# Kernel optimization log

Hardware: AMD Instinct MI355X
Metric: run time of the kernel (lower is better)

## Reference

```python
import jax, jax.numpy as jnp
import numpy as np

N = 100000
E = 300000
D = 128
EPS = 1e-5


def sage_conv(x, edge_index, Wl, bl, Wr):
    # PyG SAGEConv: out = lin_l(mean_{j in N(i)} x_j) + lin_r(x_i)
    src, dst = edge_index[0], edge_index[1]
    n = x.shape[0]
    agg = jax.ops.segment_sum(x[src], dst, num_segments=n)            # [N, d]
    cnt = jax.ops.segment_sum(jnp.ones((src.shape[0],), x.dtype), dst, num_segments=n)
    mean = agg / jnp.maximum(cnt, 1.0)[:, None]
    return mean @ Wl.T + bl + x @ Wr.T


def setup_inputs() -> dict:
    key = jax.random.key(0)
    ks = jax.random.split(key, 16)
    s = 0.05
    inp = {
        "feat": jax.random.normal(ks[0], (N, D), jnp.float32),
        "e0": jax.random.randint(ks[1], (2, E), 0, N, jnp.int32),
        "e1": jax.random.randint(ks[2], (2, E), 0, N, jnp.int32),
        "e2": jax.random.randint(ks[3], (2, E), 0, N, jnp.int32),
    }
    # per-etype SAGEConv params (in=hidden=128)
    for i, k in zip(range(3), (ks[4], ks[5], ks[6])):
        ka, kb = jax.random.split(k)
        inp[f"Wl{i}"] = jax.random.normal(ka, (D, D), jnp.float32) * s
        inp[f"bl{i}"] = jnp.zeros((D,), jnp.float32)
        inp[f"Wr{i}"] = jax.random.normal(kb, (D, D), jnp.float32) * s
    ka, kb = jax.random.split(ks[7])
    inp["Wla"] = jax.random.normal(ka, (D, D), jnp.float32) * s
    inp["bla"] = jnp.zeros((D,), jnp.float32)
    inp["Wra"] = jax.random.normal(kb, (D, D), jnp.float32) * s
    ka, kb = jax.random.split(ks[8])
    inp["Wf"] = jax.random.normal(ka, (D, D), jnp.float32) * s
    inp["bf"] = jnp.zeros((D,), jnp.float32)
    inp["Wrf"] = jax.random.normal(kb, (D, D), jnp.float32) * s
    inp["gamma"] = jnp.ones((D,), jnp.float32)
    inp["beta"] = jnp.zeros((D,), jnp.float32)
    inp["wt"] = jnp.ones((3,), jnp.float32)
    return inp


def reference(feat, Wl0, bl0, Wr0, Wl1, bl1, Wr1, Wl2, bl2, Wr2,
              Wla, bla, Wra, Wf, bf, Wrf, gamma, beta, wt, e0, e1, e2):
    out0 = sage_conv(feat, e0, Wl0, bl0, Wr0)
    out1 = sage_conv(feat, e1, Wl1, bl1, Wr1)
    out2 = sage_conv(feat, e2, Wl2, bl2, Wr2)
    all_e = jnp.concatenate([e0, e1, e2], axis=1)   # [2, 3E]
    all_out = sage_conv(feat, all_e, Wla, bla, Wra)
    comb = wt[0] * out0 + wt[1] * out1 + wt[2] * out2 + all_out
    comb = jax.nn.relu(comb)
    # BatchNorm1d (training mode: batch stats over node dim, biased var)
    mu = jnp.mean(comb, axis=0)
    var = jnp.mean((comb - mu) ** 2, axis=0)
    comb = (comb - mu) * jax.lax.rsqrt(var + EPS) * gamma + beta
    # dropout p=0.0 -> identity
    return sage_conv(comb, all_e, Wf, bf, Wrf)
```

## Files before the change

### kernel.cpp

```cpp
#include <hip/hip_runtime.h>

#define NN 100000
#define NE 300000
#define DD 128
#define NBLKG 782
#define NBLKSEG 49

typedef short bf16x8 __attribute__((ext_vector_type(8)));
typedef float f32x4 __attribute__((ext_vector_type(4)));
typedef unsigned u32x4 __attribute__((ext_vector_type(4)));

__device__ __forceinline__ unsigned short f2b(float f) {
    union { float f; unsigned u; } c; c.f = f;
    unsigned u = c.u;
    return (unsigned short)((u + 0x7fffu + ((u >> 16) & 1u)) >> 16);
}
__device__ __forceinline__ float b2lo(unsigned u) {
    union { float f; unsigned u; } c; c.u = u << 16; return c.f;
}
__device__ __forceinline__ float b2hi(unsigned u) {
    union { float f; unsigned u; } c; c.u = u & 0xffff0000u; return c.f;
}
__device__ __forceinline__ unsigned pack2(float lo, float hi) {
    return (unsigned)f2b(lo) | ((unsigned)f2b(hi) << 16);
}

__global__ __launch_bounds__(256) void feat_to_bf16(
    const float* __restrict__ feat, unsigned short* __restrict__ fb) {
    int gid = blockIdx.x * 256 + threadIdx.x;
    if (gid >= NN * 16) return;
    const f32x4* f4 = (const f32x4*)feat;
    f32x4 a = __builtin_nontemporal_load(&f4[gid * 2]);
    f32x4 b = __builtin_nontemporal_load(&f4[gid * 2 + 1]);
    uint4 o;
    o.x = pack2(a.x, a.y); o.y = pack2(a.z, a.w);
    o.z = pack2(b.x, b.y); o.w = pack2(b.z, b.w);
    ((uint4*)fb)[gid] = o;
}

__global__ __launch_bounds__(256) void prep_weights(
    const float* __restrict__ Wl0, const float* __restrict__ bl0, const float* __restrict__ Wr0,
    const float* __restrict__ Wl1, const float* __restrict__ bl1, const float* __restrict__ Wr1,
    const float* __restrict__ Wl2, const float* __restrict__ bl2, const float* __restrict__ Wr2,
    const float* __restrict__ Wla, const float* __restrict__ bla, const float* __restrict__ Wra,
    const float* __restrict__ Wf,  const float* __restrict__ bfv, const float* __restrict__ Wrf,
    const float* __restrict__ wt,
    unsigned short* __restrict__ WcatB, float* __restrict__ bias1,
    unsigned short* __restrict__ W2catB, float* __restrict__ bias2) {
    int idx = blockIdx.x * 256 + threadIdx.x;
    float w0 = wt[0], w1 = wt[1], w2 = wt[2];
    if (idx < 81920) {
        int f = idx / 640, k = idx % 640;
        float v;
        if (k < 128)      v = w0 * Wl0[f * 128 + k];
        else if (k < 256) v = w1 * Wl1[f * 128 + (k - 128)];
        else if (k < 384) v = w2 * Wl2[f * 128 + (k - 256)];
        else if (k < 512) v = Wla[f * 128 + (k - 384)];
        else {
            int kk = k - 512;
            v = w0 * Wr0[f * 128 + kk] + w1 * Wr1[f * 128 + kk] +
                w2 * Wr2[f * 128 + kk] + Wra[f * 128 + kk];
        }
        WcatB[idx] = f2b(v);
    } else if (idx < 81920 + 32768) {
        int j = idx - 81920;
        int f = j >> 8, k = j & 255;
        W2catB[j] = f2b((k < 128) ? Wf[f * 128 + k] : Wrf[f * 128 + (k - 128)]);
    } else if (idx < 81920 + 32768 + 128) {
        int f = idx - (81920 + 32768);
        bias1[f] = w0 * bl0[f] + w1 * bl1[f] + w2 * bl2[f] + bla[f];
        bias2[f] = bfv[f];
    }
}

__global__ __launch_bounds__(256) void count_deg(
    const int* __restrict__ e0, const int* __restrict__ e1, const int* __restrict__ e2,
    int* __restrict__ deg) {
    int gid = blockIdx.x * 256 + threadIdx.x;
    if (gid >= 3 * NE) return;
    int t = (gid < NE) ? 0 : ((gid < 2 * NE) ? 1 : 2);
    int i = gid - t * NE;
    const int* ep = (t == 0) ? e0 : ((t == 1) ? e1 : e2);
    atomicAdd(&deg[t * NN + ep[NE + i]], 1);
}

__global__ __launch_bounds__(256) void scan_local(
    const int* __restrict__ deg, int* __restrict__ rsloc, int* __restrict__ bsum) {
    __shared__ int sc[256];
    int b = blockIdx.x, tid = threadIdx.x;
    int seg = b / NBLKSEG, blk = b % NBLKSEG;
    int g0 = seg * NN;
    int base = blk * 2048 + tid * 8;
    int vals[8]; int tsum = 0;
#pragma unroll
    for (int j = 0; j < 8; ++j) {
        int l = base + j;
        int d = (l < NN) ? deg[g0 + l] : 0;
        vals[j] = tsum; tsum += d;
    }
    sc[tid] = tsum;
    __syncthreads();
    for (int off = 1; off < 256; off <<= 1) {
        int v = (tid >= off) ? sc[tid - off] : 0;
        __syncthreads();
        sc[tid] += v;
        __syncthreads();
    }
    int excl = sc[tid] - tsum;
#pragma unroll
    for (int j = 0; j < 8; ++j) {
        int l = base + j;
        if (l < NN) rsloc[g0 + l] = excl + vals[j];
    }
    if (tid == 255) bsum[b] = sc[255];
}

__global__ void scan_bsum(int* __restrict__ bsum) {
    int tid = threadIdx.x;
    if (tid < 3) {
        int run = 0;
        for (int b = 0; b < NBLKSEG; ++b) {
            int idx = tid * NBLKSEG + b;
            int t = bsum[idx]; bsum[idx] = run; run += t;
        }
    }
}

__global__ __launch_bounds__(256) void scan_fix(
    const int* __restrict__ deg, const int* __restrict__ rsloc, const int* __restrict__ bsum,
    int* __restrict__ fillpos, int* __restrict__ rowstartU, int* __restrict__ degall) {
    int blk = blockIdx.x, tid = threadIdx.x;
    int base = blk * 2048 + tid * 8;
    int o0 = bsum[blk], o1 = bsum[NBLKSEG + blk], o2 = bsum[2 * NBLKSEG + blk];
#pragma unroll
    for (int j = 0; j < 8; ++j) {
        int l = base + j;
        if (l < NN) {
            int d0 = deg[l], d1 = deg[NN + l], d2 = deg[2 * NN + l];
            int rU = (rsloc[l] + o0) + (rsloc[NN + l] + o1) + (rsloc[2 * NN + l] + o2);
            fillpos[l] = rU;
            fillpos[NN + l] = rU + d0;
            fillpos[2 * NN + l] = rU + d0 + d1;
            rowstartU[l] = rU;
            degall[l] = d0 + d1 + d2;
        }
    }
}

__global__ __launch_bounds__(256) void fill_csr(
    const int* __restrict__ e0, const int* __restrict__ e1, const int* __restrict__ e2,
    int* __restrict__ fillpos, int* __restrict__ csrU) {
    int gid = blockIdx.x * 256 + threadIdx.x;
    if (gid >= 3 * NE) return;
    int t = (gid < NE) ? 0 : ((gid < 2 * NE) ? 1 : 2);
    int i = gid - t * NE;
    const int* ep = (t == 0) ? e0 : ((t == 1) ? e1 : e2);
    int src = ep[i], dst = ep[NE + i];
    int p = atomicAdd(&fillpos[t * NN + dst], 1);
    csrU[p] = src;
}

__global__ __launch_bounds__(256) void gather1(
    const unsigned short* __restrict__ featB,
    const int* __restrict__ deg, const int* __restrict__ rowstartU,
    const int* __restrict__ degall, const int* __restrict__ csrU,
    unsigned short* __restrict__ meanB) {
    int n = __builtin_amdgcn_readfirstlane((int)((blockIdx.x * 256 + threadIdx.x) >> 6));
    if (n >= NN) return;
    int lane = threadIdx.x & 63;
    int d0 = deg[n], d1 = deg[NN + n];
    int dall = degall[n];
    int b1 = d0, b2 = d0 + d1;
    const int* cp = csrU + rowstartU[n];

    float p0 = 0.f, p1 = 0.f;
    float sA0 = 0.f, sA1 = 0.f;
    float sB0 = 0.f, sB1 = 0.f;

    unsigned f0 = 0, f1 = 0, f2 = 0, f3 = 0, f4 = 0;
    int i5 = 0, i6 = 0;
    {
        int i0 = 0, i1 = 0, i2 = 0, i3 = 0, i4 = 0;
        if (dall > 0) i0 = cp[0];
        if (dall > 1) i1 = cp[1];
        if (dall > 2) i2 = cp[2];
        if (dall > 3) i3 = cp[3];
        if (dall > 4) i4 = cp[4];
        if (dall > 5) i5 = cp[5];
        if (dall > 6) i6 = cp[6];
        if (dall > 0) f0 = *((const unsigned*)(featB + (size_t)i0 * DD) + lane);
        if (dall > 1) f1 = *((const unsigned*)(featB + (size_t)i1 * DD) + lane);
        if (dall > 2) f2 = *((const unsigned*)(featB + (size_t)i2 * DD) + lane);
        if (dall > 3) f3 = *((const unsigned*)(featB + (size_t)i3 * DD) + lane);
        if (dall > 4) f4 = *((const unsigned*)(featB + (size_t)i4 * DD) + lane);
    }
    for (int j = 0; j <= dall; ++j) {
        if (j == b1)   { sA0 = p0; sA1 = p1; }
        if (j == b2)   { sB0 = p0; sB1 = p1; }
        if (j == dall) break;
        unsigned u = f0;
        f0 = f1; f1 = f2; f2 = f3; f3 = f4;
        if (j + 5 < dall) f4 = *((const unsigned*)(featB + (size_t)i5 * DD) + lane);
        i5 = i6;
        if (j + 7 < dall) i6 = cp[j + 7];
        p0 += b2lo(u); p1 += b2hi(u);
    }

    int d2 = dall - b2;
    float inv0 = 1.0f / fmaxf((float)d0, 1.0f);
    float inv1 = 1.0f / fmaxf((float)d1, 1.0f);
    float inv2 = 1.0f / fmaxf((float)d2, 1.0f);
    float inva = 1.0f / fmaxf((float)dall, 1.0f);
    float m10 = sB0 - sA0, m11 = sB1 - sA1;
    float m20 = p0 - sB0,  m21 = p1 - sB1;
    unsigned* outp = (unsigned*)(meanB + (size_t)n * 512) + lane;
    __builtin_nontemporal_store(pack2(sA0 * inv0, sA1 * inv0), outp);
    __builtin_nontemporal_store(pack2(m10 * inv1, m11 * inv1), outp + 64);
    __builtin_nontemporal_store(pack2(m20 * inv2, m21 * inv2), outp + 128);
    __builtin_nontemporal_store(pack2(p0 * inva,  p1 * inva),  outp + 192);
}

__global__ __launch_bounds__(256) void gemm1_tile(
    const unsigned short* __restrict__ meanB, const unsigned short* __restrict__ featB,
    const unsigned short* __restrict__ WcatB, const float* __restrict__ bias1,
    unsigned short* __restrict__ comb, float* __restrict__ partials) {
    __shared__ unsigned short ABs[65536 / 2];
    unsigned short* As = ABs;
    unsigned short* Bs = ABs + 16384;
    int tid = threadIdx.x;
    int wid = tid >> 6, lane = tid & 63;
    int quad = lane >> 4, m16 = lane & 15;
    int nb = blockIdx.x * 128;
    int mb = (wid & 1) * 64, fb = (wid >> 1) * 64;
    f32x4 acc[4][4];
#pragma unroll
    for (int mi = 0; mi < 4; ++mi)
#pragma unroll
        for (int fi = 0; fi < 4; ++fi) acc[mi][fi] = (f32x4){0.f, 0.f, 0.f, 0.f};

    for (int kc = 0; kc < 5; ++kc) {
        __syncthreads();
#pragma unroll
        for (int it = 0; it < 8; ++it) {
            int idx = it * 256 + tid;
            int row = idx >> 4, chunk = idx & 15;
            int s = chunk >> 2, q = chunk & 3;
            int gr = min(nb + row, NN - 1);
            u32x4 v = (kc < 4)
                ? __builtin_nontemporal_load((const u32x4*)(meanB + (size_t)gr * 512 + kc * 128 + chunk * 8))
                : *(const u32x4*)(featB + (size_t)gr * DD + chunk * 8);
            *(u32x4*)&As[(((s * 128 + row) * 4) + q) * 8] = v;
        }
#pragma unroll
        for (int it = 0; it < 8; ++it) {
            int idx = it * 256 + tid;
            int f = idx >> 4, chunk = idx & 15;
            int s = chunk >> 2, q = chunk & 3;
            u32x4 v = *(const u32x4*)(WcatB + (size_t)f * 640 + kc * 128 + chunk * 8);
            *(u32x4*)&Bs[(((s * 128 + f) * 4) + q) * 8] = v;
        }
        __syncthreads();
#pragma unroll
        for (int s = 0; s < 4; ++s) {
            bf16x8 av[4], bv[4];
#pragma unroll
            for (int mi = 0; mi < 4; ++mi)
                av[mi] = *(const bf16x8*)&As[(((s * 128 + mb + mi * 16 + m16) * 4) + quad) * 8];
#pragma unroll
            for (int fi = 0; fi < 4; ++fi)
                bv[fi] = *(const bf16x8*)&Bs[(((s * 128 + fb + fi * 16 + m16) * 4) + quad) * 8];
#pragma unroll
            for (int mi = 0; mi < 4; ++mi)
#pragma unroll
                for (int fi = 0; fi < 4; ++fi)
                    acc[mi][fi] = __builtin_amdgcn_mfma_f32_16x16x32_bf16(av[mi], bv[fi], acc[mi][fi], 0, 0, 0);
        }
    }
    __syncthreads();
    float* bnS = (float*)ABs;
    float* bnQ = bnS + 128;
    if (tid < 128) { bnS[tid] = 0.f; bnQ[tid] = 0.f; }
    __syncthreads();
#pragma unroll
    for (int fi = 0; fi < 4; ++fi) {
        int f = fb + fi * 16 + m16;
        float bb = bias1[f];
        float s = 0.f, q = 0.f;
#pragma unroll
        for (int mi = 0; mi < 4; ++mi) {
#pragma unroll
            for (int r = 0; r < 4; ++r) {
                int row = nb + mb + mi * 16 + quad * 4 + r;
                float v = fmaxf(acc[mi][fi][r] + bb, 0.f);
                if (row < NN) {
                    s += v; q += v * v;
                    comb[(size_t)row * DD + f] = f2b(v);
                }
            }
        }
        atomicAdd(&bnS[f], s);
        atomicAdd(&bnQ[f], q);
    }
    __syncthreads();
    if (tid < 128) {
        partials[(size_t)tid * NBLKG + blockIdx.x] = bnS[tid];
        partials[(size_t)(128 + tid) * NBLKG + blockIdx.x] = bnQ[tid];
    }
}

__global__ __launch_bounds__(256) void bnfin(
    const float* __restrict__ partials,
    const float* __restrict__ gamma, const float* __restrict__ beta,
    float* __restrict__ bnA, float* __restrict__ bnB) {
    __shared__ float rs[256], rq[256];
    int f = blockIdx.x, tid = threadIdx.x;
    float s = 0.f, q = 0.f;
    for (int r = tid; r < NBLKG; r += 256) {
        s += partials[(size_t)f * NBLKG + r];
        q += partials[(size_t)(128 + f) * NBLKG + r];
    }
    rs[tid] = s; rq[tid] = q;
    __syncthreads();
    for (int off = 128; off > 0; off >>= 1) {
        if (tid < off) { rs[tid] += rs[tid + off]; rq[tid] += rq[tid + off]; }
        __syncthreads();
    }
    if (tid == 0) {
        float mu = rs[0] / (float)NN;
        float var = fmaxf(rq[0] / (float)NN - mu * mu, 0.f);
        float a = gamma[f] * rsqrtf(var + 1e-5f);
        bnA[f] = a;
        bnB[f] = beta[f] - mu * a;
    }
}

__global__ __launch_bounds__(256) void gather2(
    const unsigned short* __restrict__ comb,
    const int* __restrict__ rowstartU, const int* __restrict__ degall,
    const int* __restrict__ csrU,
    const float* __restrict__ bnA, const float* __restrict__ bnB,
    unsigned short* __restrict__ meanC) {
    int n = __builtin_amdgcn_readfirstlane((int)((blockIdx.x * 256 + threadIdx.x) >> 6));
    if (n >= NN) return;
    int lane = threadIdx.x & 63;
    int dall = degall[n];
    const int* cp = csrU + rowstartU[n];

    float p0 = 0.f, p1 = 0.f;
    unsigned f0 = 0, f1 = 0, f2 = 0, f3 = 0, f4 = 0;
    int i5 = 0, i6 = 0;
    {
        int i0 = 0, i1 = 0, i2 = 0, i3 = 0, i4 = 0;
        if (dall > 0) i0 = cp[0];
        if (dall > 1) i1 = cp[1];
        if (dall > 2) i2 = cp[2];
        if (dall > 3) i3 = cp[3];
        if (dall > 4) i4 = cp[4];
        if (dall > 5) i5 = cp[5];
        if (dall > 6) i6 = cp[6];
        if (dall > 0) f0 = *((const unsigned*)(comb + (size_t)i0 * DD) + lane);
        if (dall > 1) f1 = *((const unsigned*)(comb + (size_t)i1 * DD) + lane);
        if (dall > 2) f2 = *((const unsigned*)(comb + (size_t)i2 * DD) + lane);
        if (dall > 3) f3 = *((const unsigned*)(comb + (size_t)i3 * DD) + lane);
        if (dall > 4) f4 = *((const unsigned*)(comb + (size_t)i4 * DD) + lane);
    }
    for (int j = 0; j < dall; ++j) {
        unsigned u = f0;
        f0 = f1; f1 = f2; f2 = f3; f3 = f4;
        if (j + 5 < dall) f4 = *((const unsigned*)(comb + (size_t)i5 * DD) + lane);
        i5 = i6;
        if (j + 7 < dall) i6 = cp[j + 7];
        p0 += b2lo(u); p1 += b2hi(u);
    }

    float v0 = 0.f, v1 = 0.f;
    if (dall > 0) {
        float inv = 1.0f / (float)dall;
        float2 a = *(const float2*)&bnA[lane * 2];
        float2 b = *(const float2*)&bnB[lane * 2];
        v0 = a.x * (p0 * inv) + b.x;
        v1 = a.y * (p1 * inv) + b.y;
    }
    __builtin_nontemporal_store(pack2(v0, v1),
                                (unsigned*)(meanC + (size_t)n * DD) + lane);
}

__global__ __launch_bounds__(256) void gemm2_tile(
    const unsigned short* __restrict__ meanC, const unsigned short* __restrict__ comb,
    const float* __restrict__ bnA, const float* __restrict__ bnB,
    const unsigned short* __restrict__ W2catB, const float* __restrict__ bias2,
    float* __restrict__ out) {
    __shared__ unsigned short ABs[65536 / 2];
    unsigned short* As = ABs;
    unsigned short* Bs = ABs + 16384;
    int tid = threadIdx.x;
    int wid = tid >> 6, lane = tid & 63;
    int quad = lane >> 4, m16 = lane & 15;
    int nb = blockIdx.x * 128;
    int mb = (wid & 1) * 64, fb = (wid >> 1) * 64;
    f32x4 acc[4][4];
#pragma unroll
    for (int mi = 0; mi < 4; ++mi)
#pragma unroll
        for (int fi = 0; fi < 4; ++fi) acc[mi][fi] = (f32x4){0.f, 0.f, 0.f, 0.f};

    for (int kc = 0; kc < 2; ++kc) {
        __syncthreads();
#pragma unroll
        for (int it = 0; it < 8; ++it) {
            int idx = it * 256 + tid;
            int row = idx >> 4, chunk = idx & 15;
            int s = chunk >> 2, q = chunk & 3;
            int gr = min(nb + row, NN - 1);
            u32x4 v;
            if (kc == 0) {
                v = __builtin_nontemporal_load((const u32x4*)(meanC + (size_t)gr * DD + chunk * 8));
            } else {
                u32x4 c4 = *(const u32x4*)(comb + (size_t)gr * DD + chunk * 8);
                int cb = chunk * 8;
                float4 a0 = *(const float4*)&bnA[cb], a1 = *(const float4*)&bnA[cb + 4];
                float4 b0 = *(const float4*)&bnB[cb], b1 = *(const float4*)&bnB[cb + 4];
                v.x = pack2(a0.x * b2lo(c4.x) + b0.x, a0.y * b2hi(c4.x) + b0.y);
                v.y = pack2(a0.z * b2lo(c4.y) + b0.z, a0.w * b2hi(c4.y) + b0.w);
                v.z = pack2(a1.x * b2lo(c4.z) + b1.x, a1.y * b2hi(c4.z) + b1.y);
                v.w = pack2(a1.z * b2lo(c4.w) + b1.z, a1.w * b2hi(c4.w) + b1.w);
            }
            *(u32x4*)&As[(((s * 128 + row) * 4) + q) * 8] = v;
        }
#pragma unroll
        for (int it = 0; it < 8; ++it) {
            int idx = it * 256 + tid;
            int f = idx >> 4, chunk = idx & 15;
            int s = chunk >> 2, q = chunk & 3;
            u32x4 v = *(const u32x4*)(W2catB + (size_t)f * 256 + kc * 128 + chunk * 8);
            *(u32x4*)&Bs[(((s * 128 + f) * 4) + q) * 8] = v;
        }
        __syncthreads();
#pragma unroll
        for (int s = 0; s < 4; ++s) {
            bf16x8 av[4], bv[4];
#pragma unroll
            for (int mi = 0; mi < 4; ++mi)
                av[mi] = *(const bf16x8*)&As[(((s * 128 + mb + mi * 16 + m16) * 4) + quad) * 8];
#pragma unroll
            for (int fi = 0; fi < 4; ++fi)
                bv[fi] = *(const bf16x8*)&Bs[(((s * 128 + fb + fi * 16 + m16) * 4) + quad) * 8];
#pragma unroll
            for (int mi = 0; mi < 4; ++mi)
#pragma unroll
                for (int fi = 0; fi < 4; ++fi)
                    acc[mi][fi] = __builtin_amdgcn_mfma_f32_16x16x32_bf16(av[mi], bv[fi], acc[mi][fi], 0, 0, 0);
        }
    }
#pragma unroll
    for (int fi = 0; fi < 4; ++fi) {
        int f = fb + fi * 16 + m16;
        float bb = bias2[f];
#pragma unroll
        for (int mi = 0; mi < 4; ++mi) {
#pragma unroll
            for (int r = 0; r < 4; ++r) {
                int row = nb + mb + mi * 16 + quad * 4 + r;
                if (row < NN)
                    __builtin_nontemporal_store(acc[mi][fi][r] + bb,
                                                &out[(size_t)row * DD + f]);
            }
        }
    }
}

extern "C" void kernel_launch(void* const* d_in, const int* in_sizes, int n_in,
                              void* d_out, int out_size, void* d_ws, size_t ws_size,
                              hipStream_t stream) {
    const float* feat = (const float*)d_in[0];
    const int* e0 = (const int*)d_in[1];
    const int* e1 = (const int*)d_in[2];
    const int* e2 = (const int*)d_in[3];
    const float* Wl0 = (const float*)d_in[4];
    const float* bl0 = (const float*)d_in[5];
    const float* Wr0 = (const float*)d_in[6];
    const float* Wl1 = (const float*)d_in[7];
    const float* bl1 = (const float*)d_in[8];
    const float* Wr1 = (const float*)d_in[9];
    const float* Wl2 = (const float*)d_in[10];
    const float* bl2 = (const float*)d_in[11];
    const float* Wr2 = (const float*)d_in[12];
    const float* Wla = (const float*)d_in[13];
    const float* bla = (const float*)d_in[14];
    const float* Wra = (const float*)d_in[15];
    const float* Wf  = (const float*)d_in[16];
    const float* bfv = (const float*)d_in[17];
    const float* Wrf = (const float*)d_in[18];
    const float* gamma = (const float*)d_in[19];
    const float* beta  = (const float*)d_in[20];
    const float* wt    = (const float*)d_in[21];

    int* deg      = (int*)d_ws;
    int* rsloc    = deg + 3 * NN;
    int* fillpos  = rsloc + 3 * NN;
    int* csrU     = fillpos + 3 * NN;
    int* bsum     = csrU + 3 * NE;
    int* rowstartU = bsum + 160;
    int* degall    = rowstartU + NN;
    float* partials = (float*)(degall + NN);
    float* bias1  = partials + 256 * NBLKG;
    float* bias2  = bias1 + 128;
    float* bnA    = bias2 + 128;
    float* bnB    = bnA + 128;
    unsigned short* WcatB  = (unsigned short*)(bnB + 128);
    unsigned short* W2catB = WcatB + 81920;
    unsigned short* comb   = W2catB + 32768;
    unsigned short* featB  = comb + (size_t)NN * DD;
    unsigned short* meanB  = featB + (size_t)NN * DD;
    unsigned short* meanC  = meanB + (size_t)NN * 512;

    hipMemsetAsync(deg, 0, (size_t)3 * NN * sizeof(int), stream);

    feat_to_bf16<<<6250, 256, 0, stream>>>(feat, featB);
    prep_weights<<<449, 256, 0, stream>>>(Wl0, bl0, Wr0, Wl1, bl1, Wr1, Wl2, bl2, Wr2,
                                          Wla, bla, Wra, Wf, bfv, Wrf, wt,
                                          WcatB, bias1, W2catB, bias2);
    count_deg<<<3516, 256, 0, stream>>>(e0, e1, e2, deg);
    scan_local<<<147, 256, 0, stream>>>(deg, rsloc, bsum);
    scan_bsum<<<1, 64, 0, stream>>>(bsum);
    scan_fix<<<NBLKSEG, 256, 0, stream>>>(deg, rsloc, bsum, fillpos, rowstartU, degall);
    fill_csr<<<3516, 256, 0, stream>>>(e0, e1, e2, fillpos, csrU);

    gather1<<<25000, 256, 0, stream>>>(featB, deg, rowstartU, degall, csrU, meanB);
    gemm1_tile<<<NBLKG, 256, 0, stream>>>(meanB, featB, WcatB, bias1, comb, partials);
    bnfin<<<128, 256, 0, stream>>>(partials, gamma, beta, bnA, bnB);
    gather2<<<25000, 256, 0, stream>>>(comb, rowstartU, degall, csrU, bnA, bnB, meanC);
    gemm2_tile<<<NBLKG, 256, 0, stream>>>(meanC, comb, bnA, bnB, W2catB, bias2,
                                          (float*)d_out);
}
```

Before: 467.9 us.

## Merge prep kernels into one launch and XOR-swizzle GEMM LDS tiles

Fuses the feature bf16 conversion, weight preparation and degree counting into a single launch whose blocks are partitioned by blockIdx, removing two kernel launches and letting the three independent jobs overlap. Separately, both GEMM kernels switch their shared-memory A/B tiles from a k-slice-major layout to a row-major layout with an XOR swizzle on 16-byte chunks. The swizzle is meant to cut LDS bank conflicts on both the global-to-LDS stores and the MFMA operand reads. The fused kernel has heterogeneous blocks whose register use is set by the largest branch.

```diff
diff --git a/kernel.cpp b/kernel.cpp
--- a/kernel.cpp
+++ b/kernel.cpp
@@ -25,20 +25,11 @@
     return (unsigned)f2b(lo) | ((unsigned)f2b(hi) << 16);
 }
 
-__global__ __launch_bounds__(256) void feat_to_bf16(
-    const float* __restrict__ feat, unsigned short* __restrict__ fb) {
-    int gid = blockIdx.x * 256 + threadIdx.x;
-    if (gid >= NN * 16) return;
-    const f32x4* f4 = (const f32x4*)feat;
-    f32x4 a = __builtin_nontemporal_load(&f4[gid * 2]);
-    f32x4 b = __builtin_nontemporal_load(&f4[gid * 2 + 1]);
-    uint4 o;
-    o.x = pack2(a.x, a.y); o.y = pack2(a.z, a.w);
-    o.z = pack2(b.x, b.y); o.w = pack2(b.z, b.w);
-    ((uint4*)fb)[gid] = o;
-}
-
-__global__ __launch_bounds__(256) void prep_weights(
+#define NB_FEAT 6250
+#define NB_WT   449
+#define NB_DEG  3516
+__global__ __launch_bounds__(256) void prep_all(
+    const float* __restrict__ feat, unsigned short* __restrict__ fb,
     const float* __restrict__ Wl0, const float* __restrict__ bl0, const float* __restrict__ Wr0,
     const float* __restrict__ Wl1, const float* __restrict__ bl1, const float* __restrict__ Wr1,
     const float* __restrict__ Wl2, const float* __restrict__ bl2, const float* __restrict__ Wr2,
@@ -46,42 +37,53 @@
     const float* __restrict__ Wf,  const float* __restrict__ bfv, const float* __restrict__ Wrf,
     const float* __restrict__ wt,
     unsigned short* __restrict__ WcatB, float* __restrict__ bias1,
-    unsigned short* __restrict__ W2catB, float* __restrict__ bias2) {
-    int idx = blockIdx.x * 256 + threadIdx.x;
-    float w0 = wt[0], w1 = wt[1], w2 = wt[2];
-    if (idx < 81920) {
-        int f = idx / 640, k = idx % 640;
-        float v;
-        if (k < 128)      v = w0 * Wl0[f * 128 + k];
-        else if (k < 256) v = w1 * Wl1[f * 128 + (k - 128)];
-        else if (k < 384) v = w2 * Wl2[f * 128 + (k - 256)];
-        else if (k < 512) v = Wla[f * 128 + (k - 384)];
-        else {
-            int kk = k - 512;
-            v = w0 * Wr0[f * 128 + kk] + w1 * Wr1[f * 128 + kk] +
-                w2 * Wr2[f * 128 + kk] + Wra[f * 128 + kk];
-        }
-        WcatB[idx] = f2b(v);
-    } else if (idx < 81920 + 32768) {
-        int j = idx - 81920;
-        int f = j >> 8, k = j & 255;
-        W2catB[j] = f2b((k < 128) ? Wf[f * 128 + k] : Wrf[f * 128 + (k - 128)]);
-    } else if (idx < 81920 + 32768 + 128) {
-        int f = idx - (81920 + 32768);
-        bias1[f] = w0 * bl0[f] + w1 * bl1[f] + w2 * bl2[f] + bla[f];
-        bias2[f] = bfv[f];
-    }
-}
-
-__global__ __launch_bounds__(256) void count_deg(
+    unsigned short* __restrict__ W2catB, float* __restrict__ bias2,
     const int* __restrict__ e0, const int* __restrict__ e1, const int* __restrict__ e2,
     int* __restrict__ deg) {
-    int gid = blockIdx.x * 256 + threadIdx.x;
-    if (gid >= 3 * NE) return;
-    int t = (gid < NE) ? 0 : ((gid < 2 * NE) ? 1 : 2);
-    int i = gid - t * NE;
-    const int* ep = (t == 0) ? e0 : ((t == 1) ? e1 : e2);
-    atomicAdd(&deg[t * NN + ep[NE + i]], 1);
+    int b = blockIdx.x, tid = threadIdx.x;
+    if (b < NB_FEAT) {
+        int gid = b * 256 + tid;
+        if (gid >= NN * 16) return;
+        const f32x4* f4 = (const f32x4*)feat;
+        f32x4 a = __builtin_nontemporal_load(&f4[gid * 2]);
+        f32x4 c = __builtin_nontemporal_load(&f4[gid * 2 + 1]);
+        uint4 o;
+        o.x = pack2(a.x, a.y); o.y = pack2(a.z, a.w);
+        o.z = pack2(c.x, c.y); o.w = pack2(c.z, c.w);
+        ((uint4*)fb)[gid] = o;
+    } else if (b < NB_FEAT + NB_WT) {
+        int idx = (b - NB_FEAT) * 256 + tid;
+        float w0 = wt[0], w1 = wt[1], w2 = wt[2];
+        if (idx < 81920) {
+            int f = idx / 640, k = idx % 640;
+            float v;
+            if (k < 128)      v = w0 * Wl0[f * 128 + k];
+            else if (k < 256) v = w1 * Wl1[f * 128 + (k - 128)];
+            else if (k < 384) v = w2 * Wl2[f * 128 + (k - 256)];
+            else if (k < 512) v = Wla[f * 128 + (k - 384)];
+            else {
+                int kk = k - 512;
+                v = w0 * Wr0[f * 128 + kk] + w1 * Wr1[f * 128 + kk] +
+                    w2 * Wr2[f * 128 + kk] + Wra[f * 128 + kk];
+            }
+            WcatB[idx] = f2b(v);
+        } else if (idx < 81920 + 32768) {
+            int j = idx - 81920;
+            int f = j >> 8, k = j & 255;
+            W2catB[j] = f2b((k < 128) ? Wf[f * 128 + k] : Wrf[f * 128 + (k - 128)]);
+        } else if (idx < 81920 + 32768 + 128) {
+            int f = idx - (81920 + 32768);
+            bias1[f] = w0 * bl0[f] + w1 * bl1[f] + w2 * bl2[f] + bla[f];
+            bias2[f] = bfv[f];
+        }
+    } else {
+        int gid = (b - NB_FEAT - NB_WT) * 256 + tid;
+        if (gid >= 3 * NE) return;
+        int t = (gid < NE) ? 0 : ((gid < 2 * NE) ? 1 : 2);
+        int i = gid - t * NE;
+        const int* ep = (t == 0) ? e0 : ((t == 1) ? e1 : e2);
+        atomicAdd(&deg[t * NN + ep[NE + i]], 1);
+    }
 }
 
 __global__ __launch_bounds__(256) void scan_local(
@@ -244,31 +246,33 @@
         for (int it = 0; it < 8; ++it) {
             int idx = it * 256 + tid;
             int row = idx >> 4, chunk = idx & 15;
-            int s = chunk >> 2, q = chunk & 3;
             int gr = min(nb + row, NN - 1);
             u32x4 v = (kc < 4)
                 ? __builtin_nontemporal_load((const u32x4*)(meanB + (size_t)gr * 512 + kc * 128 + chunk * 8))
                 : *(const u32x4*)(featB + (size_t)gr * DD + chunk * 8);
-            *(u32x4*)&As[(((s * 128 + row) * 4) + q) * 8] = v;
+            *(u32x4*)&As[row * 128 + ((chunk ^ (row & 7)) * 8)] = v;
         }
 #pragma unroll
         for (int it = 0; it < 8; ++it) {
             int idx = it * 256 + tid;
             int f = idx >> 4, chunk = idx & 15;
-            int s = chunk >> 2, q = chunk & 3;
             u32x4 v = *(const u32x4*)(WcatB + (size_t)f * 640 + kc * 128 + chunk * 8);
-            *(u32x4*)&Bs[(((s * 128 + f) * 4) + q) * 8] = v;
+            *(u32x4*)&Bs[f * 128 + ((chunk ^ (f & 7)) * 8)] = v;
         }
         __syncthreads();
 #pragma unroll
         for (int s = 0; s < 4; ++s) {
             bf16x8 av[4], bv[4];
 #pragma unroll
-            for (int mi = 0; mi < 4; ++mi)
-                av[mi] = *(const bf16x8*)&As[(((s * 128 + mb + mi * 16 + m16) * 4) + quad) * 8];
-#pragma unroll
-            for (int fi = 0; fi < 4; ++fi)
-                bv[fi] = *(const bf16x8*)&Bs[(((s * 128 + fb + fi * 16 + m16) * 4) + quad) * 8];
+            for (int mi = 0; mi < 4; ++mi) {
+                int row = mb + mi * 16 + m16;
+                av[mi] = *(const bf16x8*)&As[row * 128 + (((s * 4 + quad) ^ (row & 7)) * 8)];
+            }
+#pragma unroll
+            for (int fi = 0; fi < 4; ++fi) {
+                int f = fb + fi * 16 + m16;
+                bv[fi] = *(const bf16x8*)&Bs[f * 128 + (((s * 4 + quad) ^ (f & 7)) * 8)];
+            }
 #pragma unroll
             for (int mi = 0; mi < 4; ++mi)
 #pragma unroll
@@ -410,7 +414,6 @@
         for (int it = 0; it < 8; ++it) {
             int idx = it * 256 + tid;
             int row = idx >> 4, chunk = idx & 15;
-            int s = chunk >> 2, q = chunk & 3;
             int gr = min(nb + row, NN - 1);
             u32x4 v;
             if (kc == 0) {
@@ -425,26 +428,29 @@
                 v.z = pack2(a1.x * b2lo(c4.z) + b1.x, a1.y * b2hi(c4.z) + b1.y);
                 v.w = pack2(a1.z * b2lo(c4.w) + b1.z, a1.w * b2hi(c4.w) + b1.w);
             }
-            *(u32x4*)&As[(((s * 128 + row) * 4) + q) * 8] = v;
+            *(u32x4*)&As[row * 128 + ((chunk ^ (row & 7)) * 8)] = v;
         }
 #pragma unroll
         for (int it = 0; it < 8; ++it) {
             int idx = it * 256 + tid;
             int f = idx >> 4, chunk = idx & 15;
-            int s = chunk >> 2, q = chunk & 3;
             u32x4 v = *(const u32x4*)(W2catB + (size_t)f * 256 + kc * 128 + chunk * 8);
-            *(u32x4*)&Bs[(((s * 128 + f) * 4) + q) * 8] = v;
+            *(u32x4*)&Bs[f * 128 + ((chunk ^ (f & 7)) * 8)] = v;
         }
         __syncthreads();
 #pragma unroll
         for (int s = 0; s < 4; ++s) {
             bf16x8 av[4], bv[4];
 #pragma unroll
-            for (int mi = 0; mi < 4; ++mi)
-                av[mi] = *(const bf16x8*)&As[(((s * 128 + mb + mi * 16 + m16) * 4) + quad) * 8];
-#pragma unroll
-            for (int fi = 0; fi < 4; ++fi)
-                bv[fi] = *(const bf16x8*)&Bs[(((s * 128 + fb + fi * 16 + m16) * 4) + quad) * 8];
+            for (int mi = 0; mi < 4; ++mi) {
+                int row = mb + mi * 16 + m16;
+                av[mi] = *(const bf16x8*)&As[row * 128 + (((s * 4 + quad) ^ (row & 7)) * 8)];
+            }
+#pragma unroll
+            for (int fi = 0; fi < 4; ++fi) {
+                int f = fb + fi * 16 + m16;
+                bv[fi] = *(const bf16x8*)&Bs[f * 128 + (((s * 4 + quad) ^ (f & 7)) * 8)];
+            }
 #pragma unroll
             for (int mi = 0; mi < 4; ++mi)
 #pragma unroll
@@ -516,11 +522,12 @@
 
     hipMemsetAsync(deg, 0, (size_t)3 * NN * sizeof(int), stream);
 
-    feat_to_bf16<<<6250, 256, 0, stream>>>(feat, featB);
-    prep_weights<<<449, 256, 0, stream>>>(Wl0, bl0, Wr0, Wl1, bl1, Wr1, Wl2, bl2, Wr2,
-                                          Wla, bla, Wra, Wf, bfv, Wrf, wt,
-                                          WcatB, bias1, W2catB, bias2);
-    count_deg<<<3516, 256, 0, stream>>>(e0, e1, e2, deg);
+    prep_all<<<NB_FEAT + NB_WT + NB_DEG, 256, 0, stream>>>(
+        feat, featB,
+        Wl0, bl0, Wr0, Wl1, bl1, Wr1, Wl2, bl2, Wr2,
+        Wla, bla, Wra, Wf, bfv, Wrf, wt,
+        WcatB, bias1, W2catB, bias2,
+        e0, e1, e2, deg);
     scan_local<<<147, 256, 0, stream>>>(deg, rsloc, bsum);
     scan_bsum<<<1, 64, 0, stream>>>(bsum);
     scan_fix<<<NBLKSEG, 256, 0, stream>>>(deg, rsloc, bsum, fillpos, rowstartU, degall);
```

After: 462.9 us. About the same (-1.1%).
